# Kernel tuning notes

Hardware: AMD Instinct MI355X
Metric: run time of the kernel (lower is better)

The kernel has to match this reference:

```python
import jax, jax.numpy as jnp
import numpy as np

SCORE_THR = 0.5
IOU_THR = 0.5
N_ANCHORS = 8400  # standard YOLO 640x640 anchor count


def setup_inputs() -> dict:
    key = jax.random.key(0)
    # [1, 5, N]: channels are (cx, cy, w, h, person_conf); uniform keeps boxes/scores in [0,1)
    yolo_raw_out = jax.random.uniform(key, (1, 5, N_ANCHORS), dtype=jnp.float32)
    return {"yolo_raw_out": yolo_raw_out}


def _pairwise_iou(b):
    # b: [N,4] xyxy
    area = (b[:, 2] - b[:, 0]) * (b[:, 3] - b[:, 1])          # [N]
    lt = jnp.maximum(b[:, None, :2], b[None, :, :2])          # [N,N,2]
    rb = jnp.minimum(b[:, None, 2:], b[None, :, 2:])          # [N,N,2]
    wh = jnp.clip(rb - lt, 0.0)
    inter = wh[..., 0] * wh[..., 1]                           # [N,N]
    union = area[:, None] + area[None, :] - inter
    return inter / jnp.maximum(union, 1e-9)


def reference(yolo_raw_out):
    # permute(0,2,1).squeeze(0) -> [N,5]
    raw = yolo_raw_out[0].T
    cx, cy, w, h = raw[:, 0], raw[:, 1], raw[:, 2], raw[:, 3]
    scores = raw[:, 4]
    # cxcywh -> xyxy (torchvision.ops.box_convert)
    xyxy = jnp.stack([cx - w / 2, cy - h / 2, cx + w / 2, cy + h / 2], axis=-1)

    valid = scores >= SCORE_THR
    # sort by score descending; invalid boxes pushed to the end
    order = jnp.argsort(-jnp.where(valid, scores, -jnp.inf))
    sb = xyxy[order]          # [N,4] sorted boxes
    ss = scores[order]        # [N]
    sv = valid[order]         # [N] score-threshold mask

    iou = _pairwise_iou(sb)   # [N,N]
    n = ss.shape[0]
    idx = jnp.arange(n)

    # Greedy NMS: in score order, an active (kept, valid) box suppresses all
    # lower-scored boxes with IoU > threshold. Faithful to torchvision.ops.nms.
    def step(keep, i):
        active = keep[i]
        suppress = (iou[i] > IOU_THR) & (idx > i) & active
        return keep & ~suppress, None

    keep, _ = jax.lax.scan(step, sv, idx)

    # Fixed-shape output: kept rows carry (x1,y1,x2,y2,score); suppressed/filtered rows zeroed.
    out = jnp.concatenate([sb, ss[:, None]], axis=1) * keep[:, None].astype(ss.dtype)
    return out
```

## Files before the change

### kernel.cpp

```cpp
#include <hip/hip_runtime.h>
#include <cstdint>

#define N_ANCH 8400
#define CBLK 132
#define SCORE_THR 0.5f

typedef unsigned long long u64;
typedef unsigned int u32;

__device__ __forceinline__ u64 sort_key(float s, int idx) {
  u32 k32 = (s >= SCORE_THR) ? ~__float_as_uint(s) : 0xFFFFFFFFu;
  return ((u64)k32 << 32) | (u32)idx;
}

__device__ __forceinline__ u64 rfl64(u64 v) {
  u32 lo = (u32)__builtin_amdgcn_readfirstlane((int)(u32)v);
  u32 hi = (u32)__builtin_amdgcn_readfirstlane((int)(u32)(v >> 32));
  return ((u64)hi << 32) | lo;
}

__global__ void __launch_bounds__(256) rank_kernel(const float* __restrict__ raw,
                                                   float4* __restrict__ sbox,
                                                   float* __restrict__ sscore) {
  #pragma clang fp contract(off)
  int tid = blockIdx.x * 256 + threadIdx.x;
  int row = tid >> 6, lane = tid & 63;
  if (row >= N_ANCH) return;
  float si = raw[4 * N_ANCH + row];
  u64 ki = sort_key(si, row);
  int cnt = 0;
  for (int j = lane; j < N_ANCH; j += 64) {
    float sj = raw[4 * N_ANCH + j];
    cnt += (sort_key(sj, j) < ki) ? 1 : 0;
  }
  #pragma unroll
  for (int d = 1; d < 64; d <<= 1) cnt += __shfl_xor(cnt, d, 64);
  if (lane == 0) {
    float cx = raw[row], cy = raw[N_ANCH + row];
    float w = raw[2 * N_ANCH + row], h = raw[3 * N_ANCH + row];
    float hw = w * 0.5f, hh = h * 0.5f;
    sbox[cnt] = make_float4(cx - hw, cy - hh, cx + hw, cy + hh);
    sscore[cnt] = si;
  }
}

__global__ void __launch_bounds__(256) mask_kernel(const float4* __restrict__ sbox,
                                                   const float* __restrict__ sscore,
                                                   u64* __restrict__ mask,
                                                   u64* __restrict__ wlo_t) {
  #pragma clang fp contract(off)
  int cb = blockIdx.x;
  int i0 = blockIdx.y * 256;
  if (cb + 5 < (i0 >> 6)) return;
  if (!(sscore[i0] >= SCORE_THR)) return;
  if (!(sscore[cb * 64] >= SCORE_THR)) return;
  int t = threadIdx.x;
  __shared__ float4 cbox[64];
  __shared__ float carea[64];
  int j0 = cb * 64;
  if (t < 64) {
    int j = j0 + t;
    float4 bj = (j < N_ANCH) ? sbox[j] : make_float4(0.f, 0.f, 0.f, 0.f);
    cbox[t] = bj;
    carea[t] = (bj.z - bj.x) * (bj.w - bj.y);
  }
  __syncthreads();
  int i = i0 + t;
  if (i >= N_ANCH) return;
  float4 bi = sbox[i];
  float ai = (bi.z - bi.x) * (bi.w - bi.y);
  u64 wHi = 0, wLo = 0;
  for (int jj = 0; jj < 64; ++jj) {
    int jg = j0 + jj;
    float4 bb = cbox[jj];
    float ltx = fmaxf(bi.x, bb.x), lty = fmaxf(bi.y, bb.y);
    float rbx = fminf(bi.z, bb.z), rby = fminf(bi.w, bb.w);
    float wx = fmaxf(rbx - ltx, 0.f), wy = fmaxf(rby - lty, 0.f);
    float inter = wx * wy;
    float uni = (ai + carea[jj]) - inter;
    float iou = inter / fmaxf(uni, 1e-9f);
    bool sup = (iou > 0.5f) && (jg < N_ANCH);
    wHi |= (u64)(sup && (jg > i)) << jj;
    wLo |= (u64)(sup && (jg < i)) << jj;
  }
  int rb = i >> 6;
  int d = rb - cb;
  if (d < 0) {
    mask[(u64)i * CBLK + cb] = wHi;
  } else if (d <= 5) {
    wlo_t[((u64)d * CBLK + rb) * 64 + (i & 63)] = wLo;
  }
}

__global__ void __launch_bounds__(512, 1) nms_kernel(const float4* __restrict__ sbox,
                                                     const float* __restrict__ sscore,
                                                     const u64* __restrict__ mask,
                                                     const u64* __restrict__ wlo_t,
                                                     float* __restrict__ out) {
  __shared__ u64 keepw[CBLK + 2];
  __shared__ u64 rem[CBLK + 2];
  int tid = threadIdx.x;
  int wave = tid >> 6, lane = tid & 63;

  float s0 = sscore[lane * 132];
  u64 pb = __ballot(s0 >= SCORE_THR);
  int cnt1 = (int)__popcll(pb);
  int n_valid = 0;
  if (cnt1 > 0) {
    int a = (cnt1 - 1) * 132 + 1;
    int i1 = a + 3 * lane;
    float t1 = (i1 + 0 < N_ANCH) ? sscore[i1 + 0] : -1.f;
    float t2 = (i1 + 1 < N_ANCH) ? sscore[i1 + 1] : -1.f;
    float t3 = (i1 + 2 < N_ANCH) ? sscore[i1 + 2] : -1.f;
    u64 q1 = __ballot(t1 >= SCORE_THR);
    u64 q2 = __ballot(t2 >= SCORE_THR);
    u64 q3 = __ballot(t3 >= SCORE_THR);
    n_valid = a + (int)__popcll(q1) + (int)__popcll(q2) + (int)__popcll(q3);
  }
  int VB = (n_valid + 63) >> 6;
  int NT = (VB + 1) >> 1;

  for (int b = tid; b < CBLK + 2; b += 512) { keepw[b] = 0; rem[b] = 0; }

  int rs = (wave - 1) * 19;
  int nr = 128 - rs; if (nr > 19) nr = 19;
  u64 tl[19], th[19];

  u64 cA=0,cB=0,cC=0,cD0=0,cD1=0,cE0=0,cE1=0,cF0=0,cF1=0,cG0=0,cG1=0;
  u64 nA=0,nB=0,nC=0,nD0=0,nD1=0,nE0=0,nE1=0,nF0=0,nF1=0,nG0=0,nG1=0;
  auto wt = [&](int d, int b) -> u64 {
    return wlo_t[((u64)d * CBLK + b) * 64 + lane];
  };
  auto load_w0 = [&](int T2, u64&A,u64&B,u64&C,u64&D0,u64&D1,u64&E0,u64&E1,
                     u64&F0,u64&F1,u64&G0,u64&G1) {
    int b0 = 2 * T2, b1 = b0 + 1;
    bool ok1 = (b1 < VB), ok2 = (b0 + 2 < VB), ok3 = (b0 + 3 < VB);
    bool ok4 = (b0 + 4 < VB), ok5 = (b0 + 5 < VB);
    A  = wt(0, b0);
    B  = ok1 ? wt(1, b1) : 0ull;
    C  = ok1 ? wt(0, b1) : 0ull;
    D0 = ok2 ? wt(2, b0 + 2) : 0ull;  D1 = ok2 ? wt(1, b0 + 2) : 0ull;
    E0 = ok3 ? wt(3, b0 + 3) : 0ull;  E1 = ok3 ? wt(2, b0 + 3) : 0ull;
    F0 = ok4 ? wt(4, b0 + 4) : 0ull;  F1 = ok4 ? wt(3, b0 + 4) : 0ull;
    G0 = ok5 ? wt(5, b0 + 5) : 0ull;  G1 = ok5 ? wt(4, b0 + 5) : 0ull;
  };

  u64 p0c = 0, p1c = 0;
  u64 q0c = 0, q1c = 0;
  u64 qn0 = 0, qn1 = 0;

  if (wave == 0 && NT > 0)
    load_w0(0, cA,cB,cC,cD0,cD1,cE0,cE1,cF0,cF1,cG0,cG1);

  for (int T = 0; T < NT; ++T) {
    asm volatile("s_waitcnt lgkmcnt(0)\ns_barrier" ::: "memory");

    if (wave == 0) {
      __builtin_amdgcn_s_setprio(1);
      int b0 = 2 * T, b1 = b0 + 1;
      u64 rb0 = rem[b0], rb1 = rem[b1];
      if (T > 0) { cA=nA; cB=nB; cC=nC; cD0=nD0; cD1=nD1; cE0=nE0; cE1=nE1;
                   cF0=nF0; cF1=nF1; cG0=nG0; cG1=nG1; }
      if (T + 1 < NT)
        load_w0(T + 1, nA,nB,nC,nD0,nD1,nE0,nE1,nF0,nF1,nG0,nG1);

      u64 remb0 = rfl64(rb0) | p0c | q0c;
      u64 remb1 = rfl64(rb1) | p1c | q1c;
      int remn0 = n_valid - b0 * 64;
      int remn1 = remn0 - 64;
      u64 vm0 = (remn0 >= 64) ? ~0ull : ((1ull << remn0) - 1ull);
      u64 vm1 = (remn1 >= 64) ? ~0ull
              : ((remn1 <= 0) ? 0ull : ((1ull << remn1) - 1ull));
      u64 act0 = vm0 & ~remb0;
      u64 act1 = vm1 & ~remb1;

      u64 U = act0, K0 = 0;
      while (U) {
        u64 covered = __ballot((cA & U) != 0ull);
        u64 nk = U & ~covered;
        u64 supp = __ballot((cA & nk) != 0ull);
        K0 |= nk;
        U &= ~(nk | supp);
      }
      u64 kw0 = K0;

      u64 s01 = __ballot((cB & kw0) != 0ull);
      u64 U1 = act1 & ~s01, K1 = 0;
      while (U1) {
        u64 covered = __ballot((cC & U1) != 0ull);
        u64 nk = U1 & ~covered;
        u64 supp = __ballot((cC & nk) != 0ull);
        K1 |= nk;
        U1 &= ~(nk | supp);
      }
      u64 kw1 = K1;

      if (lane == 0) { keepw[b0] = kw0; keepw[b1] = kw1; }

      u64 f2 = __ballot(((cD0 & kw0) | (cD1 & kw1)) != 0ull);
      u64 f3 = __ballot(((cE0 & kw0) | (cE1 & kw1)) != 0ull);
      u64 f4 = __ballot(((cF0 & kw0) | (cF1 & kw1)) != 0ull);
      u64 f5 = __ballot(((cG0 & kw0) | (cG1 & kw1)) != 0ull);
      p0c = f2; p1c = f3;
      q0c = qn0; q1c = qn1;
      qn0 = f4; qn1 = f5;
      __builtin_amdgcn_s_setprio(0);
    } else {
      if (T >= 2) {
        int u = T - 2;
        int base = 2 * u + 6;
        if (base < VB) {
          u64 acc = 0;
          #pragma unroll
          for (int r = 0; r < 19; ++r) acc |= tl[r];
          int cL = base + lane;
          if (cL < VB && acc) atomicOr((unsigned long long*)&rem[cL], acc);
          if (base + 64 < VB) {
            u64 acc2 = 0;
            #pragma unroll
            for (int r = 0; r < 19; ++r) acc2 |= th[r];
            int cH = base + 64 + lane;
            if (cH < VB && acc2) atomicOr((unsigned long long*)&rem[cH], acc2);
          }
        }
      }
      if (T >= 1 && T + 1 < NT) {
        int u = T - 1;
        int base = 2 * u + 6;
        if (base < VB) {
          u64 kws0 = rfl64(keepw[2 * u]);
          u64 kws1 = rfl64(keepw[2 * u + 1]);
          int cL = base + lane;
          bool okL = (cL < VB);
          const u64* pr = mask + (u64)(128 * u + rs) * CBLK;
          #pragma unroll
          for (int r = 0; r < 19; ++r) {
            int rr = rs + r;
            u64 kb = (rr < 64) ? (kws0 >> rr) : (kws1 >> (rr - 64));
            bool rok = (r < nr) && ((kb & 1ull) != 0ull);
            tl[r] = (rok && okL) ? pr[(u64)r * CBLK + cL] : 0ull;
          }
          if (base + 64 < VB) {
            int cH = cL + 64;
            bool okH = (cH < VB);
            #pragma unroll
            for (int r = 0; r < 19; ++r) {
              int rr = rs + r;
              u64 kb = (rr < 64) ? (kws0 >> rr) : (kws1 >> (rr - 64));
              bool rok = (r < nr) && ((kb & 1ull) != 0ull);
              th[r] = (rok && okH) ? pr[(u64)r * CBLK + cH] : 0ull;
            }
          }
        }
      }
    }
  }
  __syncthreads();

  for (int r2 = tid; r2 < N_ANCH; r2 += 512) {
    u64 kv = keepw[r2 >> 6];
    bool kp = (kv >> (r2 & 63)) & 1ull;
    float4 b4 = sbox[r2];
    float sc = sscore[r2];
    float* o = out + r2 * 5;
    o[0] = kp ? b4.x : 0.f;
    o[1] = kp ? b4.y : 0.f;
    o[2] = kp ? b4.z : 0.f;
    o[3] = kp ? b4.w : 0.f;
    o[4] = kp ? sc : 0.f;
  }
}

extern "C" void kernel_launch(void* const* d_in, const int* in_sizes, int n_in,
                              void* d_out, int out_size, void* d_ws, size_t ws_size,
                              hipStream_t stream) {
  const float* raw = (const float*)d_in[0];
  float* out = (float*)d_out;
  char* ws = (char*)d_ws;
  float4* sbox = (float4*)ws;
  float* sscore = (float*)(ws + 8448 * 16);
  u64* mask = (u64*)(ws + 8448 * 16 + 8448 * 4);
  u64* wlo_t = (u64*)(ws + 8448 * 16 + 8448 * 4 + (size_t)N_ANCH * CBLK * 8);

  rank_kernel<<<2100, 256, 0, stream>>>(raw, sbox, sscore);
  mask_kernel<<<dim3(CBLK, 33), 256, 0, stream>>>(sbox, sscore, mask, wlo_t);
  nms_kernel<<<1, 512, 0, stream>>>(sbox, sscore, mask, wlo_t, out);
}
```

Measured before the change: 147.6 us.

## Process four column blocks per NMS step and rank four rows per wave

The serial NMS loop in the single-block kernel now resolves four 64-box column blocks per barrier step instead of two. Wave 0 applies an eight-block diagonal window of suppression words, and the helper waves load and OR mask rows in the same step rather than carrying them across steps, which halves the number of barrier iterations on the serial critical path. Separately, the rank kernel now has each wave rank four anchors at once, cutting the redundant score rescans by four. In exchange, wave 0 holds more registers, helper waves do heavier per-step work, and the mask kernel writes a wider diagonal band.

```diff
diff --git a/kernel.cpp b/kernel.cpp
--- a/kernel.cpp
+++ b/kernel.cpp
@@ -4,6 +4,7 @@
 #define N_ANCH 8400
 #define CBLK 132
 #define SCORE_THR 0.5f
+#define NDIAG 8
 
 typedef unsigned long long u64;
 typedef unsigned int u32;
@@ -24,23 +25,34 @@
                                                    float* __restrict__ sscore) {
   #pragma clang fp contract(off)
   int tid = blockIdx.x * 256 + threadIdx.x;
-  int row = tid >> 6, lane = tid & 63;
-  if (row >= N_ANCH) return;
-  float si = raw[4 * N_ANCH + row];
-  u64 ki = sort_key(si, row);
-  int cnt = 0;
+  int wid = tid >> 6, lane = tid & 63;
+  int base = wid * 4;
+  float sl = raw[4 * N_ANCH + base + (lane & 3)];
+  float s0 = __shfl(sl, 0), s1 = __shfl(sl, 1);
+  float s2 = __shfl(sl, 2), s3 = __shfl(sl, 3);
+  u64 k0 = sort_key(s0, base),     k1 = sort_key(s1, base + 1);
+  u64 k2 = sort_key(s2, base + 2), k3 = sort_key(s3, base + 3);
+  int c0 = 0, c1 = 0, c2 = 0, c3 = 0;
+  #pragma unroll 2
   for (int j = lane; j < N_ANCH; j += 64) {
     float sj = raw[4 * N_ANCH + j];
-    cnt += (sort_key(sj, j) < ki) ? 1 : 0;
+    u64 kj = sort_key(sj, j);
+    c0 += kj < k0; c1 += kj < k1; c2 += kj < k2; c3 += kj < k3;
   }
   #pragma unroll
-  for (int d = 1; d < 64; d <<= 1) cnt += __shfl_xor(cnt, d, 64);
-  if (lane == 0) {
+  for (int d = 1; d < 64; d <<= 1) {
+    c0 += __shfl_xor(c0, d, 64); c1 += __shfl_xor(c1, d, 64);
+    c2 += __shfl_xor(c2, d, 64); c3 += __shfl_xor(c3, d, 64);
+  }
+  if (lane < 4) {
+    int row = base + lane;
+    int cnt = (lane == 0) ? c0 : (lane == 1) ? c1 : (lane == 2) ? c2 : c3;
+    float sc = (lane == 0) ? s0 : (lane == 1) ? s1 : (lane == 2) ? s2 : s3;
     float cx = raw[row], cy = raw[N_ANCH + row];
     float w = raw[2 * N_ANCH + row], h = raw[3 * N_ANCH + row];
     float hw = w * 0.5f, hh = h * 0.5f;
     sbox[cnt] = make_float4(cx - hw, cy - hh, cx + hw, cy + hh);
-    sscore[cnt] = si;
+    sscore[cnt] = sc;
   }
 }
 
@@ -51,7 +63,7 @@
   #pragma clang fp contract(off)
   int cb = blockIdx.x;
   int i0 = blockIdx.y * 256;
-  if (cb + 5 < (i0 >> 6)) return;
+  if (cb + 7 < (i0 >> 6)) return;
   if (!(sscore[i0] >= SCORE_THR)) return;
   if (!(sscore[cb * 64] >= SCORE_THR)) return;
   int t = threadIdx.x;
@@ -87,7 +99,7 @@
   int d = rb - cb;
   if (d < 0) {
     mask[(u64)i * CBLK + cb] = wHi;
-  } else if (d <= 5) {
+  } else if (d < NDIAG) {
     wlo_t[((u64)d * CBLK + rb) * 64 + (i & 63)] = wLo;
   }
 }
@@ -97,8 +109,8 @@
                                                      const u64* __restrict__ mask,
                                                      const u64* __restrict__ wlo_t,
                                                      float* __restrict__ out) {
-  __shared__ u64 keepw[CBLK + 2];
-  __shared__ u64 rem[CBLK + 2];
+  __shared__ u64 keepw[CBLK + 4];
+  __shared__ u64 rem[CBLK + 4];
   int tid = threadIdx.x;
   int wave = tid >> 6, lane = tid & 63;
 
@@ -118,139 +130,135 @@
     n_valid = a + (int)__popcll(q1) + (int)__popcll(q2) + (int)__popcll(q3);
   }
   int VB = (n_valid + 63) >> 6;
-  int NT = (VB + 1) >> 1;
-
-  for (int b = tid; b < CBLK + 2; b += 512) { keepw[b] = 0; rem[b] = 0; }
-
-  int rs = (wave - 1) * 19;
-  int nr = 128 - rs; if (nr > 19) nr = 19;
-  u64 tl[19], th[19];
-
-  u64 cA=0,cB=0,cC=0,cD0=0,cD1=0,cE0=0,cE1=0,cF0=0,cF1=0,cG0=0,cG1=0;
-  u64 nA=0,nB=0,nC=0,nD0=0,nD1=0,nE0=0,nE1=0,nF0=0,nF1=0,nG0=0,nG1=0;
+  int NG = (VB + 3) >> 2;
+
+  for (int b = tid; b < CBLK + 4; b += 512) { keepw[b] = 0; rem[b] = 0; }
+
+  int rs = (wave - 1) * 37;
+  int nr = 256 - rs; if (nr > 37) nr = 37;
+
+  u64 cur[26], nxt[26];
   auto wt = [&](int d, int b) -> u64 {
     return wlo_t[((u64)d * CBLK + b) * 64 + lane];
   };
-  auto load_w0 = [&](int T2, u64&A,u64&B,u64&C,u64&D0,u64&D1,u64&E0,u64&E1,
-                     u64&F0,u64&F1,u64&G0,u64&G1) {
-    int b0 = 2 * T2, b1 = b0 + 1;
-    bool ok1 = (b1 < VB), ok2 = (b0 + 2 < VB), ok3 = (b0 + 3 < VB);
-    bool ok4 = (b0 + 4 < VB), ok5 = (b0 + 5 < VB);
-    A  = wt(0, b0);
-    B  = ok1 ? wt(1, b1) : 0ull;
-    C  = ok1 ? wt(0, b1) : 0ull;
-    D0 = ok2 ? wt(2, b0 + 2) : 0ull;  D1 = ok2 ? wt(1, b0 + 2) : 0ull;
-    E0 = ok3 ? wt(3, b0 + 3) : 0ull;  E1 = ok3 ? wt(2, b0 + 3) : 0ull;
-    F0 = ok4 ? wt(4, b0 + 4) : 0ull;  F1 = ok4 ? wt(3, b0 + 4) : 0ull;
-    G0 = ok5 ? wt(5, b0 + 5) : 0ull;  G1 = ok5 ? wt(4, b0 + 5) : 0ull;
+  auto load_w0 = [&](int g, u64* R) {
+    int b = 4 * g;
+    bool k1 = (b + 1 < VB), k2 = (b + 2 < VB), k3 = (b + 3 < VB);
+    R[0] = wt(0, b);
+    R[1] = k1 ? wt(0, b + 1) : 0ull;
+    R[2] = k2 ? wt(0, b + 2) : 0ull;
+    R[3] = k3 ? wt(0, b + 3) : 0ull;
+    R[4] = k1 ? wt(1, b + 1) : 0ull;
+    R[5] = k2 ? wt(2, b + 2) : 0ull;
+    R[6] = k2 ? wt(1, b + 2) : 0ull;
+    R[7] = k3 ? wt(3, b + 3) : 0ull;
+    R[8] = k3 ? wt(2, b + 3) : 0ull;
+    R[9] = k3 ? wt(1, b + 3) : 0ull;
+    #pragma unroll
+    for (int m = 0; m < 4; ++m) {
+      int c = b + 4 + m;
+      bool ok = (c < VB);
+      #pragma unroll
+      for (int j = 0; j < 4; ++j)
+        R[10 + m * 4 + j] = ok ? wt(4 + m - j, c) : 0ull;
+    }
   };
-
-  u64 p0c = 0, p1c = 0;
-  u64 q0c = 0, q1c = 0;
-  u64 qn0 = 0, qn1 = 0;
-
-  if (wave == 0 && NT > 0)
-    load_w0(0, cA,cB,cC,cD0,cD1,cE0,cE1,cF0,cF1,cG0,cG1);
-
-  for (int T = 0; T < NT; ++T) {
+  auto fixpoint = [&](u64 colw, u64 act) -> u64 {
+    u64 U = act, K = 0;
+    while (U) {
+      u64 covered = __ballot((colw & U) != 0ull);
+      u64 nk = U & ~covered;
+      u64 supp = __ballot((colw & nk) != 0ull);
+      K |= nk;
+      U &= ~(nk | supp);
+    }
+    return K;
+  };
+
+  u64 P0 = 0, P1 = 0, P2 = 0, P3 = 0;
+
+  if (wave == 0 && NG > 0) load_w0(0, cur);
+
+  for (int g = 0; g < NG; ++g) {
     asm volatile("s_waitcnt lgkmcnt(0)\ns_barrier" ::: "memory");
 
     if (wave == 0) {
       __builtin_amdgcn_s_setprio(1);
-      int b0 = 2 * T, b1 = b0 + 1;
-      u64 rb0 = rem[b0], rb1 = rem[b1];
-      if (T > 0) { cA=nA; cB=nB; cC=nC; cD0=nD0; cD1=nD1; cE0=nE0; cE1=nE1;
-                   cF0=nF0; cF1=nF1; cG0=nG0; cG1=nG1; }
-      if (T + 1 < NT)
-        load_w0(T + 1, nA,nB,nC,nD0,nD1,nE0,nE1,nF0,nF1,nG0,nG1);
-
-      u64 remb0 = rfl64(rb0) | p0c | q0c;
-      u64 remb1 = rfl64(rb1) | p1c | q1c;
-      int remn0 = n_valid - b0 * 64;
-      int remn1 = remn0 - 64;
-      u64 vm0 = (remn0 >= 64) ? ~0ull : ((1ull << remn0) - 1ull);
-      u64 vm1 = (remn1 >= 64) ? ~0ull
-              : ((remn1 <= 0) ? 0ull : ((1ull << remn1) - 1ull));
-      u64 act0 = vm0 & ~remb0;
-      u64 act1 = vm1 & ~remb1;
-
-      u64 U = act0, K0 = 0;
-      while (U) {
-        u64 covered = __ballot((cA & U) != 0ull);
-        u64 nk = U & ~covered;
-        u64 supp = __ballot((cA & nk) != 0ull);
-        K0 |= nk;
-        U &= ~(nk | supp);
-      }
-      u64 kw0 = K0;
-
-      u64 s01 = __ballot((cB & kw0) != 0ull);
-      u64 U1 = act1 & ~s01, K1 = 0;
-      while (U1) {
-        u64 covered = __ballot((cC & U1) != 0ull);
-        u64 nk = U1 & ~covered;
-        u64 supp = __ballot((cC & nk) != 0ull);
-        K1 |= nk;
-        U1 &= ~(nk | supp);
-      }
-      u64 kw1 = K1;
-
-      if (lane == 0) { keepw[b0] = kw0; keepw[b1] = kw1; }
-
-      u64 f2 = __ballot(((cD0 & kw0) | (cD1 & kw1)) != 0ull);
-      u64 f3 = __ballot(((cE0 & kw0) | (cE1 & kw1)) != 0ull);
-      u64 f4 = __ballot(((cF0 & kw0) | (cF1 & kw1)) != 0ull);
-      u64 f5 = __ballot(((cG0 & kw0) | (cG1 & kw1)) != 0ull);
-      p0c = f2; p1c = f3;
-      q0c = qn0; q1c = qn1;
-      qn0 = f4; qn1 = f5;
+      int b = 4 * g;
+      u64 r0 = rem[b], r1 = rem[b + 1], r2 = rem[b + 2], r3 = rem[b + 3];
+      if (g > 0) {
+        #pragma unroll
+        for (int i = 0; i < 26; ++i) cur[i] = nxt[i];
+      }
+      if (g + 1 < NG) load_w0(g + 1, nxt);
+
+      int remn = n_valid - b * 64;
+      u64 vm0, vm1, vm2, vm3;
+      {
+        int m0 = remn, m1 = remn - 64, m2 = remn - 128, m3 = remn - 192;
+        vm0 = (m0 >= 64) ? ~0ull : ((m0 <= 0) ? 0ull : ((1ull << m0) - 1ull));
+        vm1 = (m1 >= 64) ? ~0ull : ((m1 <= 0) ? 0ull : ((1ull << m1) - 1ull));
+        vm2 = (m2 >= 64) ? ~0ull : ((m2 <= 0) ? 0ull : ((1ull << m2) - 1ull));
+        vm3 = (m3 >= 64) ? ~0ull : ((m3 <= 0) ? 0ull : ((1ull << m3) - 1ull));
+      }
+      u64 act0 = vm0 & ~(rfl64(r0) | P0);
+      u64 act1 = vm1 & ~(rfl64(r1) | P1);
+      u64 act2 = vm2 & ~(rfl64(r2) | P2);
+      u64 act3 = vm3 & ~(rfl64(r3) | P3);
+
+      u64 kw0 = fixpoint(cur[0], act0);
+      u64 s1 = __ballot((cur[4] & kw0) != 0ull);
+      u64 kw1 = fixpoint(cur[1], act1 & ~s1);
+      u64 s2 = __ballot(((cur[5] & kw0) | (cur[6] & kw1)) != 0ull);
+      u64 kw2 = fixpoint(cur[2], act2 & ~s2);
+      u64 s3 = __ballot(((cur[7] & kw0) | (cur[8] & kw1) | (cur[9] & kw2)) != 0ull);
+      u64 kw3 = fixpoint(cur[3], act3 & ~s3);
+
+      if (lane == 0) {
+        keepw[b] = kw0; keepw[b + 1] = kw1;
+        keepw[b + 2] = kw2; keepw[b + 3] = kw3;
+      }
+
+      P0 = __ballot(((cur[10] & kw0) | (cur[11] & kw1) |
+                     (cur[12] & kw2) | (cur[13] & kw3)) != 0ull);
+      P1 = __ballot(((cur[14] & kw0) | (cur[15] & kw1) |
+                     (cur[16] & kw2) | (cur[17] & kw3)) != 0ull);
+      P2 = __ballot(((cur[18] & kw0) | (cur[19] & kw1) |
+                     (cur[20] & kw2) | (cur[21] & kw3)) != 0ull);
+      P3 = __ballot(((cur[22] & kw0) | (cur[23] & kw1) |
+                     (cur[24] & kw2) | (cur[25] & kw3)) != 0ull);
       __builtin_amdgcn_s_setprio(0);
-    } else {
-      if (T >= 2) {
-        int u = T - 2;
-        int base = 2 * u + 6;
-        if (base < VB) {
-          u64 acc = 0;
+    } else if (g >= 1) {
+      int e = g - 1;
+      int base = 4 * e + 8;
+      if (base < VB) {
+        int wi = rs >> 6, sh = rs & 63;
+        u64 lo = keepw[4 * e + wi];
+        u64 hi = (sh + nr > 64 && wi < 3) ? keepw[4 * e + wi + 1] : 0ull;
+        u64 window = sh ? ((lo >> sh) | (hi << (64 - sh))) : lo;
+        window = rfl64(window);
+        const u64* pr = mask + (u64)(256 * e + rs) * CBLK;
+        int cL = base + lane;
+        bool okL = (cL < VB);
+        u64 acc = 0;
+        #pragma unroll
+        for (int r = 0; r < 37; ++r) {
+          bool bit = (r < nr) && (((window >> r) & 1ull) != 0ull);
+          u64 v = (bit && okL) ? pr[(u64)r * CBLK + cL] : 0ull;
+          acc |= v;
+        }
+        if (okL && acc) atomicOr((unsigned long long*)&rem[cL], acc);
+        if (base + 64 < VB) {
+          int cH = cL + 64;
+          bool okH = (cH < VB);
+          u64 acc2 = 0;
           #pragma unroll
-          for (int r = 0; r < 19; ++r) acc |= tl[r];
-          int cL = base + lane;
-          if (cL < VB && acc) atomicOr((unsigned long long*)&rem[cL], acc);
-          if (base + 64 < VB) {
-            u64 acc2 = 0;
-            #pragma unroll
-            for (int r = 0; r < 19; ++r) acc2 |= th[r];
-            int cH = base + 64 + lane;
-            if (cH < VB && acc2) atomicOr((unsigned long long*)&rem[cH], acc2);
+          for (int r = 0; r < 37; ++r) {
+            bool bit = (r < nr) && (((window >> r) & 1ull) != 0ull);
+            u64 v = (bit && okH) ? pr[(u64)r * CBLK + cH] : 0ull;
+            acc2 |= v;
           }
-        }
-      }
-      if (T >= 1 && T + 1 < NT) {
-        int u = T - 1;
-        int base = 2 * u + 6;
-        if (base < VB) {
-          u64 kws0 = rfl64(keepw[2 * u]);
-          u64 kws1 = rfl64(keepw[2 * u + 1]);
-          int cL = base + lane;
-          bool okL = (cL < VB);
-          const u64* pr = mask + (u64)(128 * u + rs) * CBLK;
-          #pragma unroll
-          for (int r = 0; r < 19; ++r) {
-            int rr = rs + r;
-            u64 kb = (rr < 64) ? (kws0 >> rr) : (kws1 >> (rr - 64));
-            bool rok = (r < nr) && ((kb & 1ull) != 0ull);
-            tl[r] = (rok && okL) ? pr[(u64)r * CBLK + cL] : 0ull;
-          }
-          if (base + 64 < VB) {
-            int cH = cL + 64;
-            bool okH = (cH < VB);
-            #pragma unroll
-            for (int r = 0; r < 19; ++r) {
-              int rr = rs + r;
-              u64 kb = (rr < 64) ? (kws0 >> rr) : (kws1 >> (rr - 64));
-              bool rok = (r < nr) && ((kb & 1ull) != 0ull);
-              th[r] = (rok && okH) ? pr[(u64)r * CBLK + cH] : 0ull;
-            }
-          }
+          if (okH && acc2) atomicOr((unsigned long long*)&rem[cH], acc2);
         }
       }
     }
@@ -282,7 +290,7 @@
   u64* mask = (u64*)(ws + 8448 * 16 + 8448 * 4);
   u64* wlo_t = (u64*)(ws + 8448 * 16 + 8448 * 4 + (size_t)N_ANCH * CBLK * 8);
 
-  rank_kernel<<<2100, 256, 0, stream>>>(raw, sbox, sscore);
+  rank_kernel<<<525, 256, 0, stream>>>(raw, sbox, sscore);
   mask_kernel<<<dim3(CBLK, 33), 256, 0, stream>>>(sbox, sscore, mask, wlo_t);
   nms_kernel<<<1, 512, 0, stream>>>(sbox, sscore, mask, wlo_t, out);
 }
```

Result: faster. 131.6 us (-10.8%).
